# Kernel tuning notes

Measured on AMD Instinct MI355X. Metric: run time of the kernel, lower is better.

The kernel has to match this reference:

```python
import jax, jax.numpy as jnp
import numpy as np

EPS = 1e-6

def _rmsnorm(x, w):
    var = jnp.mean(x * x, axis=-1, keepdims=True)
    return w * (x * jax.lax.rsqrt(var + EPS))

def _rope(t, cos, sin):
    # t: [B,S,H,d_k]; cos/sin: [S,d_k/2] -> complex multiply on (even,odd) pairs
    B, S, H, D = t.shape
    tr = t.reshape(B, S, H, D // 2, 2)
    t0, t1 = tr[..., 0], tr[..., 1]
    c = cos[None, :, None, :]
    s = sin[None, :, None, :]
    o0 = t0 * c - t1 * s
    o1 = t0 * s + t1 * c
    return jnp.stack([o0, o1], axis=-1).reshape(B, S, H, D)

def setup_inputs() -> dict:
    key = jax.random.key(0)
    ks = jax.random.split(key, 9)
    B, S, D, H, DFF = 1, 4096, 1024, 16, 4096
    dk = D // H
    hidden = int(2 * DFF / 3)  # 2730, SwiGLU hidden dim
    sc = 0.02
    x = jax.random.normal(ks[0], (B, S, D), jnp.float32)
    # RoPE tables (theta=10000)
    inv_freq = 1.0 / (10000.0 ** (np.arange(0, dk, 2, dtype=np.float32) / dk))
    ang = np.outer(np.arange(S, dtype=np.float32), inv_freq)
    freqs_cos = jnp.asarray(np.cos(ang))
    freqs_sin = jnp.asarray(np.sin(ang))
    # causal additive mask [1,1,S,S]
    mask = jnp.where(np.tril(np.ones((S, S), bool)), 0.0, -1e9).astype(jnp.float32)[None, None]
    Wq = jax.random.normal(ks[1], (D, D), jnp.float32) * sc
    Wk = jax.random.normal(ks[2], (D, D), jnp.float32) * sc
    Wv = jax.random.normal(ks[3], (D, D), jnp.float32) * sc
    Wo = jax.random.normal(ks[4], (D, D), jnp.float32) * sc
    ln1_w = jnp.ones((D,), jnp.float32)
    ln2_w = jnp.ones((D,), jnp.float32)
    w1 = jax.random.normal(ks[5], (D, hidden), jnp.float32) * sc
    w2 = jax.random.normal(ks[6], (hidden, D), jnp.float32) * sc
    w3 = jax.random.normal(ks[7], (D, hidden), jnp.float32) * sc
    return dict(x=x, freqs_cos=freqs_cos, freqs_sin=freqs_sin, mask=mask,
                Wq=Wq, Wk=Wk, Wv=Wv, Wo=Wo, ln1_w=ln1_w, ln2_w=ln2_w,
                w1=w1, w2=w2, w3=w3)

def reference(x, freqs_cos, freqs_sin, mask, Wq, Wk, Wv, Wo, ln1_w, ln2_w, w1, w2, w3):
    B, S, D = x.shape
    H = 16
    dk = D // H
    scale = jnp.sqrt(jnp.float32(dk))
    # attention sublayer (pre-RMSNorm)
    h = _rmsnorm(x, ln1_w)
    Q = (h @ Wq).reshape(B, S, H, dk)
    K = (h @ Wk).reshape(B, S, H, dk)
    V = (h @ Wv).reshape(B, S, H, dk)
    Q = _rope(Q, freqs_cos, freqs_sin)
    K = _rope(K, freqs_cos, freqs_sin)
    scores = jnp.einsum('bshd,bthd->bhst', Q, K) / scale + mask  # [B,H,S,S]
    attn = jax.nn.softmax(scores, axis=-1)
    ctx = jnp.einsum('bhst,bthd->bshd', attn, V).reshape(B, S, D)
    x = x + ctx @ Wo
    # SwiGLU FFN sublayer
    h2 = _rmsnorm(x, ln2_w)
    ff = (jax.nn.silu(h2 @ w1) * (h2 @ w3)) @ w2
    x = x + ff
    return x
```

## Files before the change

kernel.cpp:

```cpp
#include <hip/hip_runtime.h>

#define S_LEN 4096
#define D_MODEL 1024
#define NHEAD 16
#define DK 64
#define HID 2730
#define HIDP 2816
#define QKV_LD 3072

typedef unsigned short u16;
typedef unsigned int u32;
typedef __bf16 bf16x8 __attribute__((ext_vector_type(8)));
typedef float f32x4 __attribute__((ext_vector_type(4)));

#define MFMA16 __builtin_amdgcn_mfma_f32_16x16x32_bf16
#define EXP2 __builtin_amdgcn_exp2f

__device__ __forceinline__ float b2f(u16 u) {
    return __builtin_bit_cast(float, (u32)u << 16);
}
__device__ __forceinline__ u16 f2b(float f) {
    u32 u = __builtin_bit_cast(u32, f);
    u += 0x7FFF + ((u >> 16) & 1);
    return (u16)(u >> 16);
}
__device__ __forceinline__ u32 pk_trunc(float lo, float hi) {
    return __builtin_amdgcn_perm(__builtin_bit_cast(u32, hi),
                                 __builtin_bit_cast(u32, lo), 0x07060302u);
}
__device__ __forceinline__ void gll16(const u16* g, u16* l) {
    __builtin_amdgcn_global_load_lds(
        (__attribute__((address_space(1))) void*)(g),
        (__attribute__((address_space(3))) void*)(l),
        16, 0, 0);
}

__global__ __launch_bounds__(256)
void prep_k(const float* s0, const float* s1, const float* s2,
            const float* s3, const float* s4, const float* s5,
            const float* s6, u16* d0, u16* d1, u16* d2, u16* d3,
            u16* d4, u16* d5, u16* d6,
            const float* __restrict__ x, const float* __restrict__ ln1,
            u16* __restrict__ hb) {
    __shared__ float t[32][33];
    __shared__ float red[4];
    const int bid = blockIdx.x;
    const int tid = threadIdx.x;

    if (bid >= 12544) {
        const int row = bid - 12544;
        const float4 v = ((const float4*)(x + (size_t)row * D_MODEL))[tid];
        float ss = v.x * v.x + v.y * v.y + v.z * v.z + v.w * v.w;
        for (int o = 32; o; o >>= 1) ss += __shfl_down(ss, o);
        if ((tid & 63) == 0) red[tid >> 6] = ss;
        __syncthreads();
        const float tot = red[0] + red[1] + red[2] + red[3];
        const float rs = rsqrtf(tot * (1.0f / D_MODEL) + 1e-6f);
        const float4 wv = ((const float4*)ln1)[tid];
        u16* op = hb + (size_t)row * D_MODEL + tid * 4;
        u32 p0 = (u32)f2b(v.x * rs * wv.x) | ((u32)f2b(v.y * rs * wv.y) << 16);
        u32 p1 = (u32)f2b(v.z * rs * wv.z) | ((u32)f2b(v.w * rs * wv.w) << 16);
        uint2 pk; pk.x = p0; pk.y = p1;
        *(uint2*)op = pk;
        return;
    }

    const float* srcs[7] = {s0, s1, s2, s3, s4, s5, s6};
    u16* dsts[7] = {d0, d1, d2, d3, d4, d5, d6};
    const int RR[7] = {1024, 1024, 1024, 1024, 1024, 1024, 2730};
    const int CC[7] = {1024, 1024, 1024, 1024, 2730, 2730, 1024};
    const int OC[7] = {1024, 1024, 1024, 1024, 1024, 1024, 2816};
    const int XD[7] = {32, 32, 32, 32, 32, 32, 88};

    int seg, start;
    if (bid < 4096)      { seg = bid >> 10; start = seg << 10; }
    else if (bid < 6912) { seg = 4; start = 4096; }
    else if (bid < 9728) { seg = 5; start = 6912; }
    else                 { seg = 6; start = 9728; }
    const int local = bid - start;
    const int bx = local % XD[seg], byy = local / XD[seg];
    const float* in = srcs[seg];
    u16* out = dsts[seg];
    const int R = RR[seg], C = CC[seg], outC = OC[seg];

    const int r0 = byy * 32;
    const int c0 = bx * 32;
    const int tx = tid & 31, ty = tid >> 5;
#pragma unroll
    for (int j = 0; j < 4; ++j) {
        int ir = c0 + ty + j * 8;
        int ic = r0 + tx;
        t[ty + j * 8][tx] = (ir < R && ic < C) ? in[(size_t)ir * C + ic] : 0.0f;
    }
    __syncthreads();
#pragma unroll
    for (int j = 0; j < 4; ++j)
        out[(size_t)(r0 + ty + j * 8) * outC + c0 + tx] = f2b(t[tx][ty + j * 8]);
}

__global__ __launch_bounds__(256)
void rmsnorm_k(const float* __restrict__ x, const float* __restrict__ w,
               u16* __restrict__ out) {
    const int row = blockIdx.x;
    const int tid = threadIdx.x;
    const float4 v = ((const float4*)(x + (size_t)row * D_MODEL))[tid];
    float ss = v.x * v.x + v.y * v.y + v.z * v.z + v.w * v.w;
    for (int o = 32; o; o >>= 1) ss += __shfl_down(ss, o);
    __shared__ float red[4];
    if ((tid & 63) == 0) red[tid >> 6] = ss;
    __syncthreads();
    const float tot = red[0] + red[1] + red[2] + red[3];
    const float rs = rsqrtf(tot * (1.0f / D_MODEL) + 1e-6f);
    const float4 wv = ((const float4*)w)[tid];
    u16* op = out + (size_t)row * D_MODEL + tid * 4;
    u32 p0 = (u32)f2b(v.x * rs * wv.x) | ((u32)f2b(v.y * rs * wv.y) << 16);
    u32 p1 = (u32)f2b(v.z * rs * wv.z) | ((u32)f2b(v.w * rs * wv.w) << 16);
    uint2 pk; pk.x = p0; pk.y = p1;
    *(uint2*)op = pk;
}

__global__ __launch_bounds__(256)
void packkv_k(const u16* __restrict__ qkv, const float* __restrict__ fc,
              const float* __restrict__ fs, u16* __restrict__ vt,
              u16* __restrict__ kp) {
    __shared__ u16 t[32][33];
    const int h = blockIdx.z;
    const int t0 = blockIdx.x * 32;
    const int d0 = blockIdx.y * 32;
    const int tx = threadIdx.x, ty = threadIdx.y;
#pragma unroll
    for (int j = 0; j < 4; ++j)
        t[ty + j * 8][tx] =
            qkv[(size_t)(t0 + ty + j * 8) * QKV_LD + 2 * D_MODEL + h * DK + d0 + tx];

    const int id = ty * 32 + tx;
    const int sA = t0 + (id >> 3);
    const int dA = d0 + (id & 7) * 4;
    uint2 kvp = *(const uint2*)(qkv + (size_t)sA * QKV_LD + D_MODEL + h * DK + dA);
    const int fi = sA * 32 + (dA >> 1);
    const float cc0 = fc[fi], ss0 = fs[fi];
    const float cc1 = fc[fi + 1], ss1 = fs[fi + 1];
    auto rpk = [](u32 w, float c, float s) -> u32 {
        const float a = b2f((u16)w), b = b2f((u16)(w >> 16));
        return (u32)f2b(a * c - b * s) | ((u32)f2b(a * s + b * c) << 16);
    };
    kvp.x = rpk(kvp.x, cc0, ss0);
    kvp.y = rpk(kvp.y, cc1, ss1);
    *(uint2*)(kp + ((size_t)h * S_LEN + sA) * DK + dA) = kvp;

    __syncthreads();
#pragma unroll
    for (int j = 0; j < 4; ++j)
        vt[(size_t)h * DK * S_LEN + (size_t)(d0 + ty + j * 8) * S_LEN + t0 + tx] =
            t[tx][ty + j * 8];
}

template <int EPI>
__global__ __launch_bounds__(256)
void gemm128(const u16* __restrict__ A, int lda, const u16* __restrict__ Bt, int ldb,
             void* __restrict__ C, int ldc, int K, const float* __restrict__ resid) {
    const int m0 = blockIdx.y * 128, n0 = blockIdx.x * 128;
    const int tid = threadIdx.x;
    const int wave = tid >> 6, lane = tid & 63;
    const int wr = wave >> 1, wc = wave & 1;
    const int r16 = lane & 15, kq = lane >> 4;

    __shared__ __align__(16) u16 As[128 * 32];
    __shared__ __align__(16) u16 Bs[128 * 32];

    const int srow = tid >> 2, sk = (tid & 3) * 8;
    const u16* ag0 = A + (size_t)(m0 + srow) * lda + sk;
    const u16* ag1 = A + (size_t)(m0 + 64 + srow) * lda + sk;
    const u16* bg0 = Bt + (size_t)(n0 + srow) * ldb + sk;
    const u16* bg1 = Bt + (size_t)(n0 + 64 + srow) * ldb + sk;
    u16* asw = As + wave * 512;
    u16* bsw = Bs + wave * 512;

    f32x4 acc[16];
#pragma unroll
    for (int i = 0; i < 16; ++i) acc[i] = f32x4{0.f, 0.f, 0.f, 0.f};

    for (int k0 = 0; k0 < K; k0 += 32) {
        __syncthreads();
        gll16(ag0 + k0, asw);
        gll16(ag1 + k0, asw + 2048);
        gll16(bg0 + k0, bsw);
        gll16(bg1 + k0, bsw + 2048);
        __syncthreads();
        bf16x8 af[4], bf[4];
#pragma unroll
        for (int mt = 0; mt < 4; ++mt)
            af[mt] = *(const bf16x8*)&As[(wr * 64 + mt * 16 + r16) * 32 + kq * 8];
#pragma unroll
        for (int nt = 0; nt < 4; ++nt)
            bf[nt] = *(const bf16x8*)&Bs[(wc * 64 + nt * 16 + r16) * 32 + kq * 8];
#pragma unroll
        for (int mt = 0; mt < 4; ++mt)
#pragma unroll
            for (int nt = 0; nt < 4; ++nt)
                acc[mt * 4 + nt] = MFMA16(af[mt], bf[nt], acc[mt * 4 + nt], 0, 0, 0);
    }

#pragma unroll
    for (int mt = 0; mt < 4; ++mt) {
#pragma unroll
        for (int nt = 0; nt < 4; ++nt) {
            const int col = n0 + wc * 64 + nt * 16 + r16;
#pragma unroll
            for (int j = 0; j < 4; ++j) {
                const int row = m0 + wr * 64 + mt * 16 + kq * 4 + j;
                if (EPI == 0) {
                    ((u16*)C)[(size_t)row * ldc + col] = f2b(acc[mt * 4 + nt][j]);
                } else {
                    ((float*)C)[(size_t)row * ldc + col] =
                        resid[(size_t)row * ldc + col] + acc[mt * 4 + nt][j];
                }
            }
        }
    }
}

__global__ __launch_bounds__(256)
void gemm64r(const u16* __restrict__ A, int lda, const u16* __restrict__ Bt, int ldb,
             float* __restrict__ C, int ldc, int K, const float* __restrict__ resid) {
    const int m0 = blockIdx.y * 128, n0 = blockIdx.x * 64;
    const int tid = threadIdx.x;
    const int wave = tid >> 6, lane = tid & 63;
    const int r16 = lane & 15, kq = lane >> 4;

    __shared__ __align__(16) u16 As[128 * 32];
    __shared__ __align__(16) u16 Bs[64 * 32];

    const int srow = tid >> 2, sk = (tid & 3) * 8;
    const u16* ag0 = A + (size_t)(m0 + srow) * lda + sk;
    const u16* ag1 = A + (size_t)(m0 + 64 + srow) * lda + sk;
    const u16* bg = Bt + (size_t)(n0 + srow) * ldb + sk;
    u16* asw = As + wave * 512;
    u16* bsw = Bs + wave * 512;

    f32x4 acc[8];
#pragma unroll
    for (int i = 0; i < 8; ++i) acc[i] = f32x4{0.f, 0.f, 0.f, 0.f};

    for (int k0 = 0; k0 < K; k0 += 32) {
        __syncthreads();
        gll16(ag0 + k0, asw);
        gll16(ag1 + k0, asw + 2048);
        gll16(bg + k0, bsw);
        __syncthreads();
        bf16x8 af[2], bf[4];
#pragma unroll
        for (int mt = 0; mt < 2; ++mt)
            af[mt] = *(const bf16x8*)&As[(wave * 32 + mt * 16 + r16) * 32 + kq * 8];
#pragma unroll
        for (int nt = 0; nt < 4; ++nt)
            bf[nt] = *(const bf16x8*)&Bs[(nt * 16 + r16) * 32 + kq * 8];
#pragma unroll
        for (int mt = 0; mt < 2; ++mt)
#pragma unroll
            for (int nt = 0; nt < 4; ++nt)
                acc[mt * 4 + nt] = MFMA16(af[mt], bf[nt], acc[mt * 4 + nt], 0, 0, 0);
    }

#pragma unroll
    for (int mt = 0; mt < 2; ++mt)
#pragma unroll
        for (int nt = 0; nt < 4; ++nt) {
            const int col = n0 + nt * 16 + r16;
#pragma unroll
            for (int j = 0; j < 4; ++j) {
                const int row = m0 + wave * 32 + mt * 16 + kq * 4 + j;
                C[(size_t)row * ldc + col] =
                    resid[(size_t)row * ldc + col] + acc[mt * 4 + nt][j];
            }
        }
}

__global__ __launch_bounds__(256)
void gemm_dual64(const u16* __restrict__ A, int lda,
                 const u16* __restrict__ B1, const u16* __restrict__ B3, int ldb,
                 u16* __restrict__ C, int ldc, int K) {
    const int m0 = blockIdx.y * 128, n0 = blockIdx.x * 64;
    const int tid = threadIdx.x;
    const int wave = tid >> 6, lane = tid & 63;
    const int r16 = lane & 15, kq = lane >> 4;

    __shared__ __align__(16) u16 As[128 * 32];
    __shared__ __align__(16) u16 B1s[64 * 32];
    __shared__ __align__(16) u16 B3s[64 * 32];

    const int srow = tid >> 2, sk = (tid & 3) * 8;
    const u16* ag0 = A + (size_t)(m0 + srow) * lda + sk;
    const u16* ag1 = A + (size_t)(m0 + 64 + srow) * lda + sk;
    const u16* b1g = B1 + (size_t)(n0 + srow) * ldb + sk;
    const u16* b3g = B3 + (size_t)(n0 + srow) * ldb + sk;
    u16* asw = As + wave * 512;
    u16* b1w = B1s + wave * 512;
    u16* b3w = B3s + wave * 512;

    f32x4 acc1[8], acc3[8];
#pragma unroll
    for (int i = 0; i < 8; ++i) {
        acc1[i] = f32x4{0.f, 0.f, 0.f, 0.f};
        acc3[i] = f32x4{0.f, 0.f, 0.f, 0.f};
    }

    for (int k0 = 0; k0 < K; k0 += 32) {
        __syncthreads();
        gll16(ag0 + k0, asw);
        gll16(ag1 + k0, asw + 2048);
        gll16(b1g + k0, b1w);
        gll16(b3g + k0, b3w);
        __syncthreads();
        bf16x8 af[2], b1f[4], b3f[4];
#pragma unroll
        for (int mt = 0; mt < 2; ++mt)
            af[mt] = *(const bf16x8*)&As[(wave * 32 + mt * 16 + r16) * 32 + kq * 8];
#pragma unroll
        for (int nt = 0; nt < 4; ++nt) {
            b1f[nt] = *(const bf16x8*)&B1s[(nt * 16 + r16) * 32 + kq * 8];
            b3f[nt] = *(const bf16x8*)&B3s[(nt * 16 + r16) * 32 + kq * 8];
        }
#pragma unroll
        for (int mt = 0; mt < 2; ++mt)
#pragma unroll
            for (int nt = 0; nt < 4; ++nt) {
                acc1[mt * 4 + nt] = MFMA16(af[mt], b1f[nt], acc1[mt * 4 + nt], 0, 0, 0);
                acc3[mt * 4 + nt] = MFMA16(af[mt], b3f[nt], acc3[mt * 4 + nt], 0, 0, 0);
            }
    }

#pragma unroll
    for (int mt = 0; mt < 2; ++mt)
#pragma unroll
        for (int nt = 0; nt < 4; ++nt) {
            const int col = n0 + nt * 16 + r16;
#pragma unroll
            for (int j = 0; j < 4; ++j) {
                const int row = m0 + wave * 32 + mt * 16 + kq * 4 + j;
                const float v1 = acc1[mt * 4 + nt][j];
                const float v3 = acc3[mt * 4 + nt][j];
                const float sig = 1.0f / (1.0f + __expf(-v1));
                C[(size_t)row * ldc + col] = f2b(v1 * sig * v3);
            }
        }
}

__global__ __launch_bounds__(256)
void flash_k(const u16* __restrict__ qkv, const u16* __restrict__ vt,
             const u16* __restrict__ kp, const float* __restrict__ fc,
             const float* __restrict__ fs, u16* __restrict__ ctx) {
    const int h = blockIdx.x;
    const int by = blockIdx.y;
    const int hi = by >> 4, lo = by & 15;
    const int base = lo + ((hi >> 1) << 4);
    const int qi = (hi & 1) ? (63 - base) : base;
    const int q0 = qi * 64;
    const int tid = threadIdx.x;
    const int wave = tid >> 6, lane = tid & 63;
    const int r16 = lane & 15, kq = lane >> 4;

    __shared__ __align__(16) u16 Kb[2][64 * 64];
    __shared__ __align__(16) u16 Vb[2][64 * 64];
    __shared__ __align__(16) u16 Ps[4 * 16 * 64];

    const u16* kb = kp + (size_t)h * S_LEN * DK;
    const u16* vb = vt + (size_t)h * DK * S_LEN;
    const int srow = tid >> 3;
    const int lcol = ((tid & 7) ^ (srow & 7)) * 8;
    const int qloc = wave * 16 + r16;
    const int qglob = q0 + qloc;
    const int sw = r16 & 7;
    const int c0 = (kq ^ sw) * 8;
    const int c1 = ((4 ^ kq) ^ sw) * 8;
    const int psw = r16 & 14;
    u16* psrow = Ps + wave * 1024 + r16 * 64;

    const float SC = 0.125f * 1.44269504f;
    const u16* qrow = qkv + (size_t)qglob * QKV_LD + h * DK;
    uint4 uq0 = *(const uint4*)(qrow + kq * 8);
    uint4 uq1 = *(const uint4*)(qrow + 32 + kq * 8);
    const float4 c0v = *(const float4*)(fc + qglob * 32 + kq * 4);
    const float4 s0v = *(const float4*)(fs + qglob * 32 + kq * 4);
    const float4 c1v = *(const float4*)(fc + qglob * 32 + 16 + kq * 4);
    const float4 s1v = *(const float4*)(fs + qglob * 32 + 16 + kq * 4);
    auto rp = [SC](u32 w, float c, float s) -> u32 {
        const float a = b2f((u16)w), b = b2f((u16)(w >> 16));
        return (u32)f2b((a * c - b * s) * SC) |
               ((u32)f2b((a * s + b * c) * SC) << 16);
    };
    uq0.x = rp(uq0.x, c0v.x, s0v.x); uq0.y = rp(uq0.y, c0v.y, s0v.y);
    uq0.z = rp(uq0.z, c0v.z, s0v.z); uq0.w = rp(uq0.w, c0v.w, s0v.w);
    uq1.x = rp(uq1.x, c1v.x, s1v.x); uq1.y = rp(uq1.y, c1v.y, s1v.y);
    uq1.z = rp(uq1.z, c1v.z, s1v.z); uq1.w = rp(uq1.w, c1v.w, s1v.w);
    const bf16x8 qf0 = __builtin_bit_cast(bf16x8, uq0);
    const bf16x8 qf1 = __builtin_bit_cast(bf16x8, uq1);

    f32x4 o[4];
#pragma unroll
    for (int i = 0; i < 4; ++i) o[i] = f32x4{0.f, 0.f, 0.f, 0.f};
    f32x4 lacc = f32x4{0.f, 0.f, 0.f, 0.f};
    const uint4 uone = make_uint4(0x3F803F80u, 0x3F803F80u, 0x3F803F80u, 0x3F803F80u);
    const bf16x8 ones = __builtin_bit_cast(bf16x8, uone);

#pragma unroll
    for (int i = 0; i < 2; ++i) {
        const int r = srow + i * 32;
        gll16(kb + (size_t)r * DK + lcol, Kb[0] + tid * 8 + i * 2048);
        gll16(vb + (size_t)r * S_LEN + lcol, Vb[0] + tid * 8 + i * 2048);
    }

    for (int t = 0; t <= qi; ++t) {
        __syncthreads();
        if (t < qi) {
            const int t1 = (t + 1) * 64;
            u16* kd = Kb[(t + 1) & 1];
            u16* vd = Vb[(t + 1) & 1];
#pragma unroll
            for (int i = 0; i < 2; ++i) {
                const int r = srow + i * 32;
                gll16(kb + (size_t)(t1 + r) * DK + lcol, kd + tid * 8 + i * 2048);
                gll16(vb + (size_t)r * S_LEN + t1 + lcol, vd + tid * 8 + i * 2048);
            }
        }
        const u16* Ks = Kb[t & 1];
        const u16* Vs = Vb[t & 1];

        f32x4 s[4];
#pragma unroll
        for (int nt = 0; nt < 4; ++nt) {
            s[nt] = f32x4{0.f, 0.f, 0.f, 0.f};
            const bf16x8 k0 = *(const bf16x8*)&Ks[(nt * 16 + r16) * 64 + c0];
            s[nt] = MFMA16(k0, qf0, s[nt], 0, 0, 0);
            const bf16x8 k1 = *(const bf16x8*)&Ks[(nt * 16 + r16) * 64 + c1];
            s[nt] = MFMA16(k1, qf1, s[nt], 0, 0, 0);
        }

        float pr[16];
#pragma unroll
        for (int nt = 0; nt < 4; ++nt)
#pragma unroll
            for (int j = 0; j < 4; ++j) pr[nt * 4 + j] = EXP2(s[nt][j]);
        if (t == qi) {
#pragma unroll
            for (int nt = 0; nt < 4; ++nt)
#pragma unroll
                for (int j = 0; j < 4; ++j)
                    if ((nt * 16 + kq * 4 + j) > qloc) pr[nt * 4 + j] = 0.f;
        }

#pragma unroll
        for (int nt = 0; nt < 4; ++nt) {
            uint2 pk;
            pk.x = pk_trunc(pr[nt * 4 + 0], pr[nt * 4 + 1]);
            pk.y = pk_trunc(pr[nt * 4 + 2], pr[nt * 4 + 3]);
            *(uint2*)&psrow[((nt * 4 + kq) ^ psw) * 4] = pk;
        }

#pragma unroll
        for (int ks = 0; ks < 2; ++ks) {
            const bf16x8 pf = *(const bf16x8*)&psrow[((8 * ks + 2 * kq) ^ psw) * 4];
            lacc = MFMA16(ones, pf, lacc, 0, 0, 0);
            const int cv = (((ks << 2) ^ kq) ^ sw) * 8;
#pragma unroll
            for (int nt = 0; nt < 4; ++nt) {
                const bf16x8 vf = *(const bf16x8*)&Vs[(nt * 16 + r16) * 64 + cv];
                o[nt] = MFMA16(vf, pf, o[nt], 0, 0, 0);
            }
        }
    }

    const float inv = 1.0f / lacc[0];
    const size_t row = qglob;
#pragma unroll
    for (int nt = 0; nt < 4; ++nt) {
        uint2 pk;
        pk.x = (u32)f2b(o[nt][0] * inv) | ((u32)f2b(o[nt][1] * inv) << 16);
        pk.y = (u32)f2b(o[nt][2] * inv) | ((u32)f2b(o[nt][3] * inv) << 16);
        *(uint2*)&ctx[row * D_MODEL + h * DK + nt * 16 + kq * 4] = pk;
    }
}

extern "C" void kernel_launch(void* const* d_in, const int* in_sizes, int n_in,
                              void* d_out, int out_size, void* d_ws, size_t ws_size,
                              hipStream_t stream) {
    const float* x    = (const float*)d_in[0];
    const float* fcos = (const float*)d_in[1];
    const float* fsin = (const float*)d_in[2];
    const float* Wq = (const float*)d_in[4];
    const float* Wk = (const float*)d_in[5];
    const float* Wv = (const float*)d_in[6];
    const float* Wo = (const float*)d_in[7];
    const float* ln1 = (const float*)d_in[8];
    const float* ln2 = (const float*)d_in[9];
    const float* w1 = (const float*)d_in[10];
    const float* w2 = (const float*)d_in[11];
    const float* w3 = (const float*)d_in[12];
    float* out = (float*)d_out;

    char* ws = (char*)d_ws;
    size_t off = 0;
    auto alloc = [&](size_t bytes) -> char* {
        char* p = ws + off;
        off += (bytes + 255) & ~(size_t)255;
        return p;
    };
    u16* hb    = (u16*)alloc((size_t)S_LEN * D_MODEL * 2);
    u16* wqkvt = (u16*)alloc((size_t)QKV_LD * D_MODEL * 2);
    u16* wot   = (u16*)alloc((size_t)D_MODEL * D_MODEL * 2);
    u16* qkvb  = (u16*)alloc((size_t)S_LEN * QKV_LD * 2);
    u16* vt    = (u16*)alloc((size_t)S_LEN * D_MODEL * 2);
    u16* kpack = (u16*)alloc((size_t)S_LEN * D_MODEL * 2);
    u16* ctxb  = (u16*)alloc((size_t)S_LEN * D_MODEL * 2);
    float* x2  = (float*)alloc((size_t)S_LEN * D_MODEL * 4);
    u16* h2b   = (u16*)alloc((size_t)S_LEN * D_MODEL * 2);
    u16* w1t   = (u16*)alloc((size_t)HIDP * D_MODEL * 2);
    u16* w3t   = (u16*)alloc((size_t)HIDP * D_MODEL * 2);
    u16* w2t   = (u16*)alloc((size_t)D_MODEL * HIDP * 2);
    u16* ffb   = (u16*)alloc((size_t)S_LEN * HIDP * 2);

    const dim3 tb32(32, 8);

    prep_k<<<16640, 256, 0, stream>>>(
        Wq, Wk, Wv, Wo, w1, w3, w2,
        wqkvt, wqkvt + (size_t)D_MODEL * D_MODEL,
        wqkvt + (size_t)2 * D_MODEL * D_MODEL, wot, w1t, w3t, w2t,
        x, ln1, hb);

    gemm128<0><<<dim3(QKV_LD / 128, S_LEN / 128), 256, 0, stream>>>(
        hb, D_MODEL, wqkvt, D_MODEL, qkvb, QKV_LD, D_MODEL, nullptr);

    packkv_k<<<dim3(S_LEN / 32, DK / 32, NHEAD), tb32, 0, stream>>>(
        qkvb, fcos, fsin, vt, kpack);

    flash_k<<<dim3(NHEAD, 64), 256, 0, stream>>>(qkvb, vt, kpack, fcos, fsin, ctxb);

    gemm64r<<<dim3(D_MODEL / 64, S_LEN / 128), 256, 0, stream>>>(
        ctxb, D_MODEL, wot, D_MODEL, x2, D_MODEL, D_MODEL, x);

    rmsnorm_k<<<S_LEN, 256, 0, stream>>>(x2, ln2, h2b);

    gemm_dual64<<<dim3(HIDP / 64, S_LEN / 128), 256, 0, stream>>>(
        h2b, D_MODEL, w1t, w3t, D_MODEL, ffb, HIDP, D_MODEL);

    gemm64r<<<dim3(D_MODEL / 64, S_LEN / 128), 256, 0, stream>>>(
        ffb, HIDP, w2t, HIDP, out, D_MODEL, HIDP, x2);
}
```

Measured before the change: 414.4 us.

## Widen SwiGLU dual GEMM tile to 128x96 with 2x2 wave layout

The fused w1/w3 GEMM now uses 96-wide N tiles, and its four waves are arranged 2x2, each computing a 64x48 subtile, instead of 32x64 strips. The hidden padding grows from 2816 to 2880 so it divides by 96, and the weight-prep grid is adjusted to match. B1 and B3 tiles share one LDS buffer, and the loads are split across three global-to-LDS copies. The aim is more MFMA work per loaded byte and fewer blocks. The cost is more accumulator registers (occupancy hint of 3) and extra padded columns in both the FFN GEMM and the w2 GEMM.

```diff
diff --git a/kernel.cpp b/kernel.cpp
--- a/kernel.cpp
+++ b/kernel.cpp
@@ -5,7 +5,7 @@
 #define NHEAD 16
 #define DK 64
 #define HID 2730
-#define HIDP 2816
+#define HIDP 2880
 #define QKV_LD 3072
 
 typedef unsigned short u16;
@@ -47,8 +47,8 @@
     const int bid = blockIdx.x;
     const int tid = threadIdx.x;
 
-    if (bid >= 12544) {
-        const int row = bid - 12544;
+    if (bid >= 12736) {
+        const int row = bid - 12736;
         const float4 v = ((const float4*)(x + (size_t)row * D_MODEL))[tid];
         float ss = v.x * v.x + v.y * v.y + v.z * v.z + v.w * v.w;
         for (int o = 32; o; o >>= 1) ss += __shfl_down(ss, o);
@@ -69,14 +69,14 @@
     u16* dsts[7] = {d0, d1, d2, d3, d4, d5, d6};
     const int RR[7] = {1024, 1024, 1024, 1024, 1024, 1024, 2730};
     const int CC[7] = {1024, 1024, 1024, 1024, 2730, 2730, 1024};
-    const int OC[7] = {1024, 1024, 1024, 1024, 1024, 1024, 2816};
-    const int XD[7] = {32, 32, 32, 32, 32, 32, 88};
+    const int OC[7] = {1024, 1024, 1024, 1024, 1024, 1024, 2880};
+    const int XD[7] = {32, 32, 32, 32, 32, 32, 90};
 
     int seg, start;
     if (bid < 4096)      { seg = bid >> 10; start = seg << 10; }
-    else if (bid < 6912) { seg = 4; start = 4096; }
-    else if (bid < 9728) { seg = 5; start = 6912; }
-    else                 { seg = 6; start = 9728; }
+    else if (bid < 6976) { seg = 4; start = 4096; }
+    else if (bid < 9856) { seg = 5; start = 6976; }
+    else                 { seg = 6; start = 9856; }
     const int local = bid - start;
     const int bx = local % XD[seg], byy = local / XD[seg];
     const float* in = srcs[seg];
@@ -276,70 +276,76 @@
         }
 }
 
-__global__ __launch_bounds__(256)
-void gemm_dual64(const u16* __restrict__ A, int lda,
+__global__ __launch_bounds__(256, 3)
+void gemm_dual96(const u16* __restrict__ A, int lda,
                  const u16* __restrict__ B1, const u16* __restrict__ B3, int ldb,
                  u16* __restrict__ C, int ldc, int K) {
-    const int m0 = blockIdx.y * 128, n0 = blockIdx.x * 64;
+    const int m0 = blockIdx.y * 128, n0 = blockIdx.x * 96;
     const int tid = threadIdx.x;
     const int wave = tid >> 6, lane = tid & 63;
+    const int wr = wave >> 1, wc = wave & 1;
     const int r16 = lane & 15, kq = lane >> 4;
 
     __shared__ __align__(16) u16 As[128 * 32];
-    __shared__ __align__(16) u16 B1s[64 * 32];
-    __shared__ __align__(16) u16 B3s[64 * 32];
+    __shared__ __align__(16) u16 Bs[192 * 32];
 
     const int srow = tid >> 2, sk = (tid & 3) * 8;
     const u16* ag0 = A + (size_t)(m0 + srow) * lda + sk;
     const u16* ag1 = A + (size_t)(m0 + 64 + srow) * lda + sk;
-    const u16* b1g = B1 + (size_t)(n0 + srow) * ldb + sk;
-    const u16* b3g = B3 + (size_t)(n0 + srow) * ldb + sk;
-    u16* asw = As + wave * 512;
-    u16* b1w = B1s + wave * 512;
-    u16* b3w = B3s + wave * 512;
-
-    f32x4 acc1[8], acc3[8];
-#pragma unroll
-    for (int i = 0; i < 8; ++i) {
+    const u16* bp0 = B1 + (size_t)(n0 + srow) * ldb + sk;
+    const u16* bp1 = (srow < 32)
+        ? B1 + (size_t)(n0 + 64 + srow) * ldb + sk
+        : B3 + (size_t)(n0 + srow - 32) * ldb + sk;
+    const u16* bp2 = B3 + (size_t)(n0 + 32 + srow) * ldb + sk;
+    u16* asw0 = As + wave * 512;
+    u16* asw1 = As + 2048 + wave * 512;
+    u16* bsw0 = Bs + wave * 512;
+    u16* bsw1 = Bs + 2048 + wave * 512;
+    u16* bsw2 = Bs + 4096 + wave * 512;
+
+    f32x4 acc1[12], acc3[12];
+#pragma unroll
+    for (int i = 0; i < 12; ++i) {
         acc1[i] = f32x4{0.f, 0.f, 0.f, 0.f};
         acc3[i] = f32x4{0.f, 0.f, 0.f, 0.f};
     }
 
     for (int k0 = 0; k0 < K; k0 += 32) {
         __syncthreads();
-        gll16(ag0 + k0, asw);
-        gll16(ag1 + k0, asw + 2048);
-        gll16(b1g + k0, b1w);
-        gll16(b3g + k0, b3w);
-        __syncthreads();
-        bf16x8 af[2], b1f[4], b3f[4];
-#pragma unroll
-        for (int mt = 0; mt < 2; ++mt)
-            af[mt] = *(const bf16x8*)&As[(wave * 32 + mt * 16 + r16) * 32 + kq * 8];
-#pragma unroll
-        for (int nt = 0; nt < 4; ++nt) {
-            b1f[nt] = *(const bf16x8*)&B1s[(nt * 16 + r16) * 32 + kq * 8];
-            b3f[nt] = *(const bf16x8*)&B3s[(nt * 16 + r16) * 32 + kq * 8];
-        }
-#pragma unroll
-        for (int mt = 0; mt < 2; ++mt)
-#pragma unroll
-            for (int nt = 0; nt < 4; ++nt) {
-                acc1[mt * 4 + nt] = MFMA16(af[mt], b1f[nt], acc1[mt * 4 + nt], 0, 0, 0);
-                acc3[mt * 4 + nt] = MFMA16(af[mt], b3f[nt], acc3[mt * 4 + nt], 0, 0, 0);
+        gll16(ag0 + k0, asw0);
+        gll16(ag1 + k0, asw1);
+        gll16(bp0 + k0, bsw0);
+        gll16(bp1 + k0, bsw1);
+        gll16(bp2 + k0, bsw2);
+        __syncthreads();
+        bf16x8 af[4], b1f[3], b3f[3];
+#pragma unroll
+        for (int mt = 0; mt < 4; ++mt)
+            af[mt] = *(const bf16x8*)&As[(wr * 64 + mt * 16 + r16) * 32 + kq * 8];
+#pragma unroll
+        for (int nt = 0; nt < 3; ++nt) {
+            b1f[nt] = *(const bf16x8*)&Bs[(wc * 48 + nt * 16 + r16) * 32 + kq * 8];
+            b3f[nt] = *(const bf16x8*)&Bs[(96 + wc * 48 + nt * 16 + r16) * 32 + kq * 8];
+        }
+#pragma unroll
+        for (int mt = 0; mt < 4; ++mt)
+#pragma unroll
+            for (int nt = 0; nt < 3; ++nt) {
+                acc1[mt * 3 + nt] = MFMA16(af[mt], b1f[nt], acc1[mt * 3 + nt], 0, 0, 0);
+                acc3[mt * 3 + nt] = MFMA16(af[mt], b3f[nt], acc3[mt * 3 + nt], 0, 0, 0);
             }
     }
 
 #pragma unroll
-    for (int mt = 0; mt < 2; ++mt)
-#pragma unroll
-        for (int nt = 0; nt < 4; ++nt) {
-            const int col = n0 + nt * 16 + r16;
+    for (int mt = 0; mt < 4; ++mt)
+#pragma unroll
+        for (int nt = 0; nt < 3; ++nt) {
+            const int col = n0 + wc * 48 + nt * 16 + r16;
 #pragma unroll
             for (int j = 0; j < 4; ++j) {
-                const int row = m0 + wave * 32 + mt * 16 + kq * 4 + j;
-                const float v1 = acc1[mt * 4 + nt][j];
-                const float v3 = acc3[mt * 4 + nt][j];
+                const int row = m0 + wr * 64 + mt * 16 + kq * 4 + j;
+                const float v1 = acc1[mt * 3 + nt][j];
+                const float v3 = acc3[mt * 3 + nt][j];
                 const float sig = 1.0f / (1.0f + __expf(-v1));
                 C[(size_t)row * ldc + col] = f2b(v1 * sig * v3);
             }
@@ -521,7 +527,7 @@
 
     const dim3 tb32(32, 8);
 
-    prep_k<<<16640, 256, 0, stream>>>(
+    prep_k<<<16832, 256, 0, stream>>>(
         Wq, Wk, Wv, Wo, w1, w3, w2,
         wqkvt, wqkvt + (size_t)D_MODEL * D_MODEL,
         wqkvt + (size_t)2 * D_MODEL * D_MODEL, wot, w1t, w3t, w2t,
@@ -540,7 +546,7 @@
 
     rmsnorm_k<<<S_LEN, 256, 0, stream>>>(x2, ln2, h2b);
 
-    gemm_dual64<<<dim3(HIDP / 64, S_LEN / 128), 256, 0, stream>>>(
+    gemm_dual96<<<dim3(HIDP / 96, S_LEN / 128), 256, 0, stream>>>(
         h2b, D_MODEL, w1t, w3t, D_MODEL, ffb, HIDP, D_MODEL);
 
     gemm64r<<<dim3(D_MODEL / 64, S_LEN / 128), 256, 0, stream>>>(
```

Measured after the change: 416.4 us. Within noise of the previous version (+0.5%).
